# Kernel optimization log

Hardware: AMD Instinct MI355X
Metric: run time of the kernel (lower is better)

Reference implementation:

```python
import jax, jax.numpy as jnp
import numpy as np

BLOCK_SIZE = 8
SELECT_TOPK = 32
HIDDEN = 512
CHANNELS = 384
NUM_HEADS = 8
B, H, W = 8, 64, 64


def setup_inputs() -> dict:
    key = jax.random.key(0)
    ks = jax.random.split(key, 8)
    num_block_tot = (H // BLOCK_SIZE) * (W // BLOCK_SIZE)
    bs2 = BLOCK_SIZE * BLOCK_SIZE
    x = jax.random.normal(ks[0], (B, H, W, CHANNELS), dtype=jnp.float32)
    aw = jax.random.normal(ks[1], (NUM_HEADS, B, num_block_tot, bs2, bs2 + SELECT_TOPK), dtype=jnp.float32)
    attn_weights = jax.nn.softmax(aw, axis=-1)  # module expects sum(-1)==1
    weights = jax.random.uniform(ks[2], (B, num_block_tot, SELECT_TOPK), dtype=jnp.float32)
    indexes = jax.random.randint(ks[3], (B, num_block_tot, SELECT_TOPK), 0, H * W)
    in_proj_w = jax.random.normal(ks[4], (3 * HIDDEN, CHANNELS), dtype=jnp.float32) * 0.02
    in_proj_b = jax.random.normal(ks[5], (3 * HIDDEN,), dtype=jnp.float32) * 0.02
    out_proj_w = jax.random.normal(ks[6], (CHANNELS, HIDDEN), dtype=jnp.float32) * 0.02
    out_proj_b = jax.random.normal(ks[7], (CHANNELS,), dtype=jnp.float32) * 0.02
    return {"x": x, "attn_weights": attn_weights, "weights": weights,
            "in_proj_w": in_proj_w, "in_proj_b": in_proj_b,
            "out_proj_w": out_proj_w, "out_proj_b": out_proj_b,
            "indexes": indexes}


def reference(x, attn_weights, weights, in_proj_w, in_proj_b, out_proj_w, out_proj_b, indexes):
    batch, height, width, _ = x.shape
    bsz = BLOCK_SIZE
    nbh, nbw = height // bsz, width // bsz
    nbt = nbh * nbw
    num_heads = attn_weights.shape[0]
    hid = HIDDEN
    hd = hid // num_heads
    topk = SELECT_TOPK

    proj = jnp.einsum('bhwc,oc->bhwo', x, in_proj_w) + in_proj_b  # (B,H,W,3*hid)
    s, xh, y = jnp.split(proj, 3, axis=-1)
    xh = xh * jnp.tanh(s)  # Balancer/Whiten/Identity are identity in fwd

    # top-k gathered tokens: (B, nbt, topk, hid) without (B,nbt,num_tokens,hid) blowup
    x_flat = xh.reshape(batch, height * width, hid)
    sel = jax.vmap(lambda xf, ix: xf[ix])(x_flat, indexes)  # (B,nbt,topk,hid)
    sel = sel * weights[..., None]
    sel = sel.reshape(batch, nbt, topk, num_heads, hd).transpose(3, 0, 1, 2, 4)  # (nh,B,nbt,topk,hd)

    # block-local tokens: (nh, B, nbt, bsz^2, hd)
    blk = xh.reshape(batch, nbh, bsz, nbw, bsz, num_heads, hd)
    blk = blk.transpose(5, 0, 1, 3, 2, 4, 6).reshape(num_heads, batch, nbt, bsz * bsz, hd)

    kv = jnp.concatenate([blk, sel], axis=3)  # (nh,B,nbt,bsz^2+topk,hd)
    out = jnp.einsum('hbnqk,hbnkd->hbnqd', attn_weights, kv)  # (nh,B,nbt,bsz^2,hd)

    out = out.reshape(num_heads, batch, nbh, nbw, bsz, bsz, hd)
    out = out.transpose(1, 2, 4, 3, 5, 0, 6).reshape(batch, height, width, hid)
    out = out * y
    return jnp.einsum('bhwd,cd->bhwc', out, out_proj_w) + out_proj_b
```

## Files before the change

### kernel.cpp

```cpp
#include <hip/hip_runtime.h>
#include <hip/hip_bf16.h>
#include <stdint.h>

#define CH   384
#define HID  512
#define NHD  8
#define MTOT 32768

typedef __attribute__((ext_vector_type(8))) short bf16x8;
typedef __attribute__((ext_vector_type(4))) float f32x4;
typedef unsigned short u16;

__device__ __forceinline__ float bf2f(u16 v){ return __uint_as_float(((unsigned)v)<<16); }
__device__ __forceinline__ u16 f2bf(float f){
  unsigned u = __float_as_uint(f);
  return (u16)((u + 0x7fffu + ((u>>16)&1u)) >> 16);
}
__device__ __forceinline__ float fast_tanh(float s){
  float e = __expf(2.f*s);
  return 1.f - 2.f*__builtin_amdgcn_rcpf(e + 1.f);
}
__device__ __forceinline__ void gload_lds16(const void* g, void* l){
  __builtin_amdgcn_global_load_lds((const __attribute__((address_space(1))) void*)g,
                                   (__attribute__((address_space(3))) void*)l, 16, 0, 0);
}

#define CVT_N1 (MTOT*CH/4)
#define CVT_N2 (3*HID*CH/4)
#define CVT_N3 (CH*HID/4)
__global__ void k_cvt3(const float* __restrict__ x,  u16* __restrict__ xo,
                       const float* __restrict__ w1, u16* __restrict__ w1o,
                       const float* __restrict__ w2, u16* __restrict__ w2o){
  const int total = CVT_N1 + CVT_N2 + CVT_N3;
  int i = blockIdx.x*blockDim.x + threadIdx.x;
  int stride = gridDim.x*blockDim.x;
  for (; i < total; i += stride){
    const float4* src; ushort4* dst; int k;
    if (i < CVT_N1){ src = (const float4*)x;  dst = (ushort4*)xo;  k = i; }
    else if (i < CVT_N1 + CVT_N2){ src = (const float4*)w1; dst = (ushort4*)w1o; k = i - CVT_N1; }
    else { src = (const float4*)w2; dst = (ushort4*)w2o; k = i - CVT_N1 - CVT_N2; }
    float4 v = src[k];
    ushort4 o; o.x=f2bf(v.x); o.y=f2bf(v.y); o.z=f2bf(v.z); o.w=f2bf(v.w);
    dst[k] = o;
  }
}

__global__ __launch_bounds__(256)
void k_gemm1(const u16* __restrict__ xb, const u16* __restrict__ w1b,
             const float* __restrict__ b1,
             u16* __restrict__ xh, u16* __restrict__ yb)
{
  __shared__ short lds[14336];
  const int tid = threadIdx.x;
  const int w = tid >> 6, lw = tid & 63;
  const int bid = blockIdx.x;
  const int xcd = bid & 7, ii = bid >> 3;
  const int m0 = (xcd*32 + (ii >> 4)) * 128;
  const int h0 = (ii & 15) * 32;
  const int lc = lw & 15, lk = lw >> 4;

  f32x4 acc[2][6] = {};

  const int sl = (lw & 7) ^ (lw >> 3);
  const int rsub = lw >> 3;
  const u16* gsrc[7]; int ldst[7];
  #pragma unroll
  for (int i = 0; i < 7; ++i){
    int c = w*7 + i;
    if (c < 16){
      int r = c*8 + rsub;
      gsrc[i] = xb + (size_t)(m0 + r)*CH + sl*8;
      ldst[i] = c*512;
    } else {
      int rb = (c-16)*8 + rsub;
      int grow = (rb >> 5)*HID + h0 + (rb & 31);
      gsrc[i] = w1b + (size_t)grow*CH + sl*8;
      ldst[i] = 8192 + (c-16)*512;
    }
  }

  #pragma unroll 1
  for (int kt = 0; kt < 6; ++kt){
    #pragma unroll
    for (int i = 0; i < 7; ++i)
      gload_lds16(gsrc[i] + kt*64, &lds[ldst[i]]);
    __syncthreads();
    #pragma unroll
    for (int ks = 0; ks < 2; ++ks){
      const int s = (ks*4 + lk) ^ (lc & 7);
      bf16x8 af[2], bfr[6];
      #pragma unroll
      for (int mi = 0; mi < 2; ++mi){
        int row = w*32 + mi*16 + lc;
        af[mi] = *(const bf16x8*)&lds[row*64 + s*8];
      }
      #pragma unroll
      for (int nj = 0; nj < 6; ++nj){
        int row = nj*16 + lc;
        bfr[nj] = *(const bf16x8*)&lds[8192 + row*64 + s*8];
      }
      #pragma unroll
      for (int mi = 0; mi < 2; ++mi)
        #pragma unroll
        for (int nj = 0; nj < 6; ++nj)
          acc[mi][nj] = __builtin_amdgcn_mfma_f32_16x16x32_bf16(af[mi], bfr[nj], acc[mi][nj], 0,0,0);
    }
    __syncthreads();
  }

  {
    short* epx = &lds[w*2560];
    short* epy = &lds[w*2560 + 1280];
    float bs[2], bx[2], by[2];
    #pragma unroll
    for (int f = 0; f < 2; ++f){
      int col = h0 + f*16 + lc;
      bs[f] = b1[col]; bx[f] = b1[512 + col]; by[f] = b1[1024 + col];
    }
    #pragma unroll
    for (int mi = 0; mi < 2; ++mi)
      #pragma unroll
      for (int f = 0; f < 2; ++f)
        #pragma unroll
        for (int j = 0; j < 4; ++j){
          float sv = acc[mi][0+f][j] + bs[f];
          float xv = (acc[mi][2+f][j] + bx[f]) * fast_tanh(sv);
          float yv = acc[mi][4+f][j] + by[f];
          int row = mi*16 + lk*4 + j;
          epx[row*40 + f*16 + lc] = (short)f2bf(xv);
          epy[row*40 + f*16 + lc] = (short)f2bf(yv);
        }
    __syncthreads();
    const int row = lw >> 1, half = lw & 1;
    const size_t gbase = (size_t)(m0 + w*32 + row)*HID + h0 + half*16;
    #pragma unroll
    for (int q = 0; q < 2; ++q){
      bf16x8 v = *(const bf16x8*)&epx[row*40 + half*16 + q*8];
      *(bf16x8*)&xh[gbase + q*8] = v;
    }
    #pragma unroll
    for (int q = 0; q < 2; ++q){
      bf16x8 v = *(const bf16x8*)&epy[row*40 + half*16 + q*8];
      *(bf16x8*)&yb[gbase + q*8] = v;
    }
  }
}

__global__ __launch_bounds__(256)
void k_attn(const float* __restrict__ aw, const float* __restrict__ wts,
            const int* __restrict__ idxs,
            const u16* __restrict__ xh, const u16* __restrict__ yb,
            u16* __restrict__ zb)
{
  __shared__ short ldsb[6144 + 12288];
  short* lKv = ldsb;
  float* lAw = (float*)&ldsb[6144];
  const int tid0 = threadIdx.x;
  const int w = tid0 >> 6, lane = tid0 & 63;
  const int bid = blockIdx.x;
  const int h = bid >> 9;
  const int b = (bid >> 6) & 7;
  const int n = bid & 63;
  const int bh = n >> 3, bw = n & 7;

  {
    const float* awt = aw + (size_t)bid * 6144;
    #pragma unroll
    for (int i = 0; i < 6; ++i){
      int c = i*4 + w;
      int s = c*64 + lane;
      int row = s / 24;
      int sir = s - row*24;
      int src = row*24 + (sir ^ (row & 7));
      gload_lds16(awt + src*4, (char*)lAw + (size_t)c*1024);
    }
  }

  {
    const int dg = tid0 & 7;
    {
      int pair = tid0 >> 3;
      int t0 = pair*2;
      int pix = (bh*8 + (t0>>3))*64 + bw*8 + (t0&7);
      size_t r0 = (size_t)b*4096 + pix, r1 = r0 + 1;
      bf16x8 v0 = *(const bf16x8*)&xh[r0*HID + h*64 + dg*8];
      bf16x8 v1 = *(const bf16x8*)&xh[r1*HID + h*64 + dg*8];
      #pragma unroll
      for (int j = 0; j < 8; ++j){
        int d = dg*8 + j;
        int elem = (d*96 + t0) ^ (dg<<3);
        unsigned pk = (unsigned)(u16)v0[j] | ((unsigned)(u16)v1[j] << 16);
        *(unsigned*)&lKv[elem] = pk;
      }
    }
    if (tid0 < 128){
      int pr = tid0 >> 3;
      int t0 = 64 + pr*2;
      int e = (b*64+n)*32 + pr*2;
      size_t r0 = (size_t)b*4096 + idxs[e];
      size_t r1 = (size_t)b*4096 + idxs[e+1];
      bf16x8 v0 = *(const bf16x8*)&xh[r0*HID + h*64 + dg*8];
      bf16x8 v1 = *(const bf16x8*)&xh[r1*HID + h*64 + dg*8];
      #pragma unroll
      for (int j = 0; j < 8; ++j){
        int d = dg*8 + j;
        int elem = (d*96 + t0) ^ (dg<<3);
        unsigned pk = (unsigned)(u16)v0[j] | ((unsigned)(u16)v1[j] << 16);
        *(unsigned*)&lKv[elem] = pk;
      }
    }
  }

  float wv[8];
  {
    const float* wp = wts + (size_t)(b*64+n)*32 + (lane>>4)*8;
    float4 a = *(const float4*)wp, c = *(const float4*)(wp+4);
    wv[0]=a.x; wv[1]=a.y; wv[2]=a.z; wv[3]=a.w;
    wv[4]=c.x; wv[5]=c.y; wv[6]=c.z; wv[7]=c.w;
  }
  bf16x8 yv0, yv1;
  const int yq = tid0 >> 2, yc = tid0 & 3;
  {
    int pix = (bh*8 + (yq>>3))*64 + bw*8 + (yq&7);
    const u16* yrow = yb + ((size_t)b*4096 + pix)*HID + h*64 + yc*16;
    yv0 = *(const bf16x8*)&yrow[0];
    yv1 = *(const bf16x8*)&yrow[8];
  }
  __syncthreads();

  const int lc = lane & 15, lk = lane >> 4;
  f32x4 acc[4] = {};
  #pragma unroll
  for (int ks = 0; ks < 3; ++ks){
    bf16x8 af;
    {
      int r = w*16 + lc;
      int sr = ks*8 + lk*2;
      int key = r & 7;
      float4 f0 = *(const float4*)&lAw[(r*24 + (sr ^ key))*4];
      float4 f1 = *(const float4*)&lAw[(r*24 + ((sr+1) ^ key))*4];
      float t[8] = {f0.x,f0.y,f0.z,f0.w,f1.x,f1.y,f1.z,f1.w};
      #pragma unroll
      for (int j = 0; j < 8; ++j){
        float v = (ks == 2) ? t[j]*wv[j] : t[j];
        af[j] = (short)f2bf(v);
      }
    }
    bf16x8 bv[4];
    #pragma unroll
    for (int nj = 0; nj < 4; ++nj){
      int d = nj*16 + lc;
      int idx = (d*96 + ks*32 + lk*8) ^ ((d>>3)<<3);
      bv[nj] = *(const bf16x8*)&lKv[idx];
    }
    #pragma unroll
    for (int nj = 0; nj < 4; ++nj)
      acc[nj] = __builtin_amdgcn_mfma_f32_16x16x32_bf16(af, bv[nj], acc[nj], 0,0,0);
  }
  __syncthreads();

  *(bf16x8*)&lKv[yq*72 + yc*16    ] = yv0;
  *(bf16x8*)&lKv[yq*72 + yc*16 + 8] = yv1;

  #pragma unroll
  for (int nj = 0; nj < 4; ++nj){
    int d = nj*16 + lc;
    size_t gcol = (size_t)h*64 + d;
    #pragma unroll
    for (int j = 0; j < 4; ++j){
      int q = w*16 + lk*4 + j;
      int pix = (bh*8 + (q>>3))*64 + bw*8 + (q&7);
      size_t r = (size_t)b*4096 + pix;
      float yvf = bf2f((u16)lKv[q*72 + d]);
      zb[r*HID + gcol] = f2bf(acc[nj][j] * yvf);
    }
  }
}

__global__ __launch_bounds__(256)
void k_gemm2(const u16* __restrict__ zb, const u16* __restrict__ w2b,
             const float* __restrict__ b2, float* __restrict__ out)
{
  __shared__ short lds[16384];
  const int tid = threadIdx.x;
  const int w = tid>>6, lw = tid&63;
  const int wm = w>>1, wn = w&1;
  const int bid = blockIdx.x;
  const int xcd = bid & 7, ii = bid >> 3;
  const int m0 = (xcd*32 + ii/3) * 128;
  const int n0 = (ii%3) * 128;
  const int lc = lw & 15, lk = lw >> 4;

  f32x4 acc[4][4] = {};

  const int sl_g = (lw & 3) ^ ((lw >> 3) & 3);
  const int rsub = lw >> 2;
  const u16* gsrc[4]; int ldst[4];
  #pragma unroll
  for (int i = 0; i < 4; ++i){
    int c = w*4 + i;
    if (c < 8){
      int r = c*16 + rsub;
      gsrc[i] = zb + (size_t)(m0+r)*HID + sl_g*8;
      ldst[i] = c*512;
    } else {
      int cb = c - 8;
      int r = cb*16 + rsub;
      gsrc[i] = w2b + (size_t)(n0+r)*HID + sl_g*8;
      ldst[i] = 4096 + cb*512;
    }
  }
  auto STAGE = [&](int buf, int kt){
    #pragma unroll
    for (int i = 0; i < 4; ++i)
      gload_lds16(gsrc[i] + kt*32, &lds[ldst[i] + buf*8192]);
  };
  const int skey = (lc >> 1) & 3;
  auto COMPUTE = [&](int buf){
    const short* pa = lds + buf*8192;
    const short* pb = lds + buf*8192 + 4096;
    bf16x8 af[4], bb[4];
    #pragma unroll
    for (int mi=0; mi<4; ++mi){
      int row = wm*64 + mi*16 + lc;
      af[mi] = *(const bf16x8*)&pa[row*32 + (lk ^ skey)*8];
    }
    #pragma unroll
    for (int nj=0; nj<4; ++nj){
      int row = wn*64 + nj*16 + lc;
      bb[nj] = *(const bf16x8*)&pb[row*32 + (lk ^ skey)*8];
    }
    #pragma unroll
    for (int mi=0; mi<4; ++mi)
      #pragma unroll
      for (int nj=0; nj<4; ++nj)
        acc[mi][nj] = __builtin_amdgcn_mfma_f32_16x16x32_bf16(af[mi], bb[nj], acc[mi][nj], 0,0,0);
  };

  STAGE(0, 0);
  #pragma unroll 1
  for (int kt = 0; kt < 16; ++kt){
    if (kt < 15){
      STAGE((kt+1)&1, kt+1);
      asm volatile("s_waitcnt vmcnt(4)" ::: "memory");
    } else {
      asm volatile("s_waitcnt vmcnt(0)" ::: "memory");
    }
    __builtin_amdgcn_sched_barrier(0);
    __builtin_amdgcn_s_barrier();
    COMPUTE(kt&1);
    __builtin_amdgcn_sched_barrier(0);
    __builtin_amdgcn_s_barrier();
  }

  const int lr4 = lk*4;
  #pragma unroll
  for (int nj=0; nj<4; ++nj){
    int col = n0 + wn*64 + nj*16 + lc;
    float bias = b2[col];
    #pragma unroll
    for (int mi=0; mi<4; ++mi){
      #pragma unroll
      for (int j=0; j<4; ++j){
        int row = m0 + wm*64 + mi*16 + lr4 + j;
        out[(size_t)row*CH + col] = acc[mi][nj][j] + bias;
      }
    }
  }
}

extern "C" void kernel_launch(void* const* d_in, const int* in_sizes, int n_in,
                              void* d_out, int out_size, void* d_ws, size_t ws_size,
                              hipStream_t stream) {
  const float* x   = (const float*)d_in[0];
  const float* aw  = (const float*)d_in[1];
  const float* wts = (const float*)d_in[2];
  const float* w1  = (const float*)d_in[3];
  const float* b1  = (const float*)d_in[4];
  const float* w2  = (const float*)d_in[5];
  const float* b2  = (const float*)d_in[6];
  const int*   idx = (const int*)d_in[7];
  float* out = (float*)d_out;

  char* ws = (char*)d_ws;
  u16* x_bf  = (u16*)(ws);
  u16* w1_bf = (u16*)(ws + 25165824);
  u16* w2_bf = (u16*)(ws + 26345472);
  u16* xh_bf = (u16*)(ws + 26738688);
  u16* y_bf  = (u16*)(ws + 60293120);
  u16* z_bf  = (u16*)(ws + 93847552);

  k_cvt3<<<2048, 256, 0, stream>>>(x, x_bf, w1, w1_bf, w2, w2_bf);

  k_gemm1<<<4096, 256, 0, stream>>>(x_bf, w1_bf, b1, xh_bf, y_bf);
  k_attn<<<NHD*8*64, 256, 0, stream>>>(aw, wts, idx, xh_bf, y_bf, z_bf);
  k_gemm2<<<768, 256, 0, stream>>>(z_bf, w2_bf, b2, out);
}
```

Measured before the change: 135.5 us.

## Switch GEMM2 to single-buffered 64-wide K tiles and drop epilogue barrier

The output-projection GEMM drops its double-buffered 32-wide K pipeline and uses a single LDS buffer with 64-wide K tiles. Each tile is loaded, followed by a barrier, two MFMA sub-steps, and another barrier. This halves the number of loop iterations and barriers but stops overlapping global loads with compute. Separately, the __syncthreads between the LDS epilogue writes and reads in the first GEMM is removed. Those reads may still be safe without it, but only if each wave reads only rows it wrote itself, so this needs checking for a race.

Measured after the change: 137.4 us. About the same (+1.4%).

```diff
diff --git a/kernel.cpp b/kernel.cpp
--- a/kernel.cpp
+++ b/kernel.cpp
@@ -130,7 +130,6 @@
           epx[row*40 + f*16 + lc] = (short)f2bf(xv);
           epy[row*40 + f*16 + lc] = (short)f2bf(yv);
         }
-    __syncthreads();
     const int row = lw >> 1, half = lw & 1;
     const size_t gbase = (size_t)(m0 + w*32 + row)*HID + h0 + half*16;
     #pragma unroll
@@ -293,75 +292,62 @@
 
   f32x4 acc[4][4] = {};
 
-  const int sl_g = (lw & 3) ^ ((lw >> 3) & 3);
-  const int rsub = lw >> 2;
-  const u16* gsrc[4]; int ldst[4];
-  #pragma unroll
-  for (int i = 0; i < 4; ++i){
-    int c = w*4 + i;
-    if (c < 8){
-      int r = c*16 + rsub;
-      gsrc[i] = zb + (size_t)(m0+r)*HID + sl_g*8;
+  const int sl = (lw & 7) ^ (lw >> 3);
+  const int rsub = lw >> 3;
+  const u16* gsrc[8]; int ldst[8];
+  #pragma unroll
+  for (int i = 0; i < 8; ++i){
+    int c = w*8 + i;
+    if (c < 16){
+      int r = c*8 + rsub;
+      gsrc[i] = zb + (size_t)(m0 + r)*HID + sl*8;
       ldst[i] = c*512;
     } else {
-      int cb = c - 8;
-      int r = cb*16 + rsub;
-      gsrc[i] = w2b + (size_t)(n0+r)*HID + sl_g*8;
-      ldst[i] = 4096 + cb*512;
-    }
-  }
-  auto STAGE = [&](int buf, int kt){
-    #pragma unroll
-    for (int i = 0; i < 4; ++i)
-      gload_lds16(gsrc[i] + kt*32, &lds[ldst[i] + buf*8192]);
-  };
-  const int skey = (lc >> 1) & 3;
-  auto COMPUTE = [&](int buf){
-    const short* pa = lds + buf*8192;
-    const short* pb = lds + buf*8192 + 4096;
-    bf16x8 af[4], bb[4];
-    #pragma unroll
-    for (int mi=0; mi<4; ++mi){
-      int row = wm*64 + mi*16 + lc;
-      af[mi] = *(const bf16x8*)&pa[row*32 + (lk ^ skey)*8];
-    }
-    #pragma unroll
-    for (int nj=0; nj<4; ++nj){
-      int row = wn*64 + nj*16 + lc;
-      bb[nj] = *(const bf16x8*)&pb[row*32 + (lk ^ skey)*8];
-    }
-    #pragma unroll
-    for (int mi=0; mi<4; ++mi)
-      #pragma unroll
-      for (int nj=0; nj<4; ++nj)
-        acc[mi][nj] = __builtin_amdgcn_mfma_f32_16x16x32_bf16(af[mi], bb[nj], acc[mi][nj], 0,0,0);
-  };
-
-  STAGE(0, 0);
+      int cb = c - 16;
+      int r = cb*8 + rsub;
+      gsrc[i] = w2b + (size_t)(n0 + r)*HID + sl*8;
+      ldst[i] = 8192 + cb*512;
+    }
+  }
+
   #pragma unroll 1
-  for (int kt = 0; kt < 16; ++kt){
-    if (kt < 15){
-      STAGE((kt+1)&1, kt+1);
-      asm volatile("s_waitcnt vmcnt(4)" ::: "memory");
-    } else {
-      asm volatile("s_waitcnt vmcnt(0)" ::: "memory");
-    }
-    __builtin_amdgcn_sched_barrier(0);
-    __builtin_amdgcn_s_barrier();
-    COMPUTE(kt&1);
-    __builtin_amdgcn_sched_barrier(0);
-    __builtin_amdgcn_s_barrier();
+  for (int kt = 0; kt < 8; ++kt){
+    #pragma unroll
+    for (int i = 0; i < 8; ++i)
+      gload_lds16(gsrc[i] + kt*64, &lds[ldst[i]]);
+    __syncthreads();
+    #pragma unroll
+    for (int ks = 0; ks < 2; ++ks){
+      const int s = (ks*4 + lk) ^ (lc & 7);
+      bf16x8 af[4], bb[4];
+      #pragma unroll
+      for (int mi = 0; mi < 4; ++mi){
+        int row = wm*64 + mi*16 + lc;
+        af[mi] = *(const bf16x8*)&lds[row*64 + s*8];
+      }
+      #pragma unroll
+      for (int nj = 0; nj < 4; ++nj){
+        int row = wn*64 + nj*16 + lc;
+        bb[nj] = *(const bf16x8*)&lds[8192 + row*64 + s*8];
+      }
+      #pragma unroll
+      for (int mi = 0; mi < 4; ++mi)
+        #pragma unroll
+        for (int nj = 0; nj < 4; ++nj)
+          acc[mi][nj] = __builtin_amdgcn_mfma_f32_16x16x32_bf16(af[mi], bb[nj], acc[mi][nj], 0,0,0);
+    }
+    __syncthreads();
   }
 
   const int lr4 = lk*4;
   #pragma unroll
-  for (int nj=0; nj<4; ++nj){
+  for (int nj = 0; nj < 4; ++nj){
     int col = n0 + wn*64 + nj*16 + lc;
     float bias = b2[col];
     #pragma unroll
-    for (int mi=0; mi<4; ++mi){
-      #pragma unroll
-      for (int j=0; j<4; ++j){
+    for (int mi = 0; mi < 4; ++mi){
+      #pragma unroll
+      for (int j = 0; j < 4; ++j){
         int row = m0 + wm*64 + mi*16 + lr4 + j;
         out[(size_t)row*CH + col] = acc[mi][nj][j] + bias;
       }
```
